# Kernel tuning notes

Measured on AMD Instinct MI355X. Metric: run time of the kernel, lower is better.

Reference implementation:

```python
import jax, jax.numpy as jnp
import numpy as np

N = 50000      # nodes
E = 800000     # edges (avg degree 16)
IN = 256       # input feature dim
H = 128        # hidden dim
L = 2          # num layers
R = 8          # NUM_RELS_WITH_MASK
RD = 16        # rel_emb_dim
CONF_W = 0.5   # conf_log_weight
LN_EPS = 1e-5


def setup_inputs() -> dict:
    key = jax.random.key(0)
    ks = jax.random.split(key, 12)
    x = jax.random.normal(ks[0], (N, IN), dtype=jnp.float32)
    edge_index = jax.random.randint(ks[1], (2, E), 0, N, dtype=jnp.int32)
    edge_type = jax.random.randint(ks[2], (E,), 0, R, dtype=jnp.int32)
    edge_attr = jax.random.uniform(ks[3], (E, 1), dtype=jnp.float32)
    # encoder input projection (Linear with bias)
    W_in = jax.random.normal(ks[4], (IN, H), dtype=jnp.float32) / np.sqrt(IN)
    b_in = jnp.zeros((H,), dtype=jnp.float32)
    # per-layer params, stacked on leading L dim
    W_msg = jax.random.normal(ks[5], (L, H, H), dtype=jnp.float32) / np.sqrt(H)
    rel_emb = jax.random.normal(ks[6], (L, R, RD), dtype=jnp.float32)
    W_rel = jax.random.normal(ks[7], (L, RD, H), dtype=jnp.float32) / np.sqrt(RD)
    att_vec = jax.random.normal(ks[8], (L, 3 * H), dtype=jnp.float32) / np.sqrt(3 * H)
    bias = jnp.zeros((L, H), dtype=jnp.float32)
    ln_g = jnp.ones((L, H), dtype=jnp.float32)
    ln_b = jnp.zeros((L, H), dtype=jnp.float32)
    return {"x": x, "edge_index": edge_index, "edge_type": edge_type,
            "edge_attr": edge_attr, "W_in": W_in, "b_in": b_in,
            "W_msg": W_msg, "rel_emb": rel_emb, "W_rel": W_rel,
            "att_vec": att_vec, "bias": bias, "ln_g": ln_g, "ln_b": ln_b}


def _layer_norm(h, g, b):
    mu = jnp.mean(h, axis=-1, keepdims=True)
    var = jnp.mean(jnp.square(h - mu), axis=-1, keepdims=True)
    return (h - mu) * jax.lax.rsqrt(var + LN_EPS) * g + b


def reference(x, edge_index, edge_type, edge_attr,
              W_in, b_in, W_msg, rel_emb, W_rel, att_vec, bias, ln_g, ln_b):
    src, dst = edge_index[0], edge_index[1]
    t = jnp.clip(edge_type, 0, R - 1)
    log_conf = CONF_W * jnp.log(jnp.maximum(edge_attr[:, 0], 1e-6))  # [E]

    h = jax.nn.relu(x @ W_in + b_in)  # [N,H]
    for l in range(L):
        # project on nodes first (same math as projecting gathered rows, E >> N)
        hm = h @ W_msg[l]                 # [N,H]
        h_src = hm[src]                   # [E,H]
        h_dst = hm[dst]                   # [E,H]
        r = rel_emb[l][t] @ W_rel[l]      # [E,H]
        a = att_vec[l]
        a_d, a_s, a_r = a[:H], a[H:2 * H], a[2 * H:]
        e = h_dst @ a_d + h_src @ a_s + r @ a_r          # [E]
        e = jax.nn.leaky_relu(e, negative_slope=0.2) + log_conf
        # segment softmax grouped by dst
        m = jax.ops.segment_max(e, dst, num_segments=N)  # [N]
        ex = jnp.exp(e - m[dst])
        s = jax.ops.segment_sum(ex, dst, num_segments=N)  # [N]
        alpha = ex / s[dst]                               # [E]
        msg = h_src * alpha[:, None]                      # [E,H]
        out = jax.ops.segment_sum(msg, dst, num_segments=N) + bias[l]
        h = _layer_norm(h + jax.nn.relu(out), ln_g[l], ln_b[l])
    return h
```

## Files before the change

kernel.cpp:

```cpp
#include <hip/hip_runtime.h>
#include <hip/hip_bf16.h>

#define N_NODES 50000
#define NE      800000
#define IN_DIM  256
#define H_DIM   128
#define NL      2
#define NR      8
#define RD_DIM  16
#define CONF_W  0.5f
#define LN_EPS  1e-5f

#define SCAN_CHUNK 1024
#define NB_SCAN    ((N_NODES + SCAN_CHUNK - 1) / SCAN_CHUNK)

typedef __attribute__((ext_vector_type(8))) short bf16x8;
typedef __attribute__((ext_vector_type(4))) float f32x4;

__device__ __forceinline__ unsigned short f2bf(float f) {
    unsigned u = __float_as_uint(f);
    u += 0x7fffu + ((u >> 16) & 1u);
    return (unsigned short)(u >> 16);
}
__device__ __forceinline__ float bf2f(unsigned short v) {
    return __uint_as_float(((unsigned)v) << 16);
}


__global__ void k_zero_counts(int* __restrict__ counts) {
    int i = blockIdx.x * 256 + threadIdx.x;
    if (i < N_NODES) counts[i] = 0;
}

__global__ void k_count(const int* __restrict__ dstv, int* __restrict__ counts,
                        int* __restrict__ rank) {
    int i = blockIdx.x * 256 + threadIdx.x;
    if (i >= NE) return;
    rank[i] = atomicAdd(counts + dstv[i], 1);
}

__global__ __launch_bounds__(256) void k_scan1(const int* __restrict__ counts,
                                               int* __restrict__ bsum) {
    __shared__ int lsum[256];
    const int t = threadIdx.x, b = blockIdx.x;
    const int base = b * SCAN_CHUNK + t * 4;
    int s = 0;
#pragma unroll
    for (int j = 0; j < 4; ++j) {
        int idx = base + j;
        if (idx < N_NODES) s += counts[idx];
    }
    lsum[t] = s;
    __syncthreads();
    for (int off = 128; off; off >>= 1) {
        if (t < off) lsum[t] += lsum[t + off];
        __syncthreads();
    }
    if (t == 0) bsum[b] = lsum[0];
}

__global__ void k_scan2(const int* __restrict__ bsum, int* __restrict__ bbase) {
    int lane = threadIdx.x & 63;
    int v = (lane < NB_SCAN) ? bsum[lane] : 0;
    int inc = v;
    for (int off = 1; off < 64; off <<= 1) {
        int tmp = __shfl_up(inc, off);
        if (lane >= off) inc += tmp;
    }
    if (lane < NB_SCAN) bbase[lane] = inc - v;
}

__global__ __launch_bounds__(256) void k_scan3(const int* __restrict__ counts,
                                               const int* __restrict__ bbase,
                                               int* __restrict__ offsets) {
    __shared__ int lsum[256];
    const int t = threadIdx.x, b = blockIdx.x;
    const int base = b * SCAN_CHUNK + t * 4;
    int c[4];
    int s = 0;
#pragma unroll
    for (int j = 0; j < 4; ++j) {
        int idx = base + j;
        c[j] = (idx < N_NODES) ? counts[idx] : 0;
        s += c[j];
    }
    lsum[t] = s;
    __syncthreads();
    for (int off = 1; off < 256; off <<= 1) {
        int v = (t >= off) ? lsum[t - off] : 0;
        __syncthreads();
        lsum[t] += v;
        __syncthreads();
    }
    int run = bbase[b] + lsum[t] - s;
#pragma unroll
    for (int j = 0; j < 4; ++j) {
        int idx = base + j;
        if (idx < N_NODES) { offsets[idx] = run; run += c[j]; }
    }
}

__global__ void k_perm(const int* __restrict__ srcv, const int* __restrict__ dstv,
                       const int* __restrict__ et, const float* __restrict__ ea,
                       const int* __restrict__ offsets, const int* __restrict__ rank,
                       int* __restrict__ src_sorted, int* __restrict__ type_sorted,
                       float* __restrict__ lc_sorted) {
    int i = blockIdx.x * 256 + threadIdx.x;
    if (i >= NE) return;
    int p = offsets[dstv[i]] + rank[i];
    src_sorted[p] = srcv[i];
    int t = et[i]; t = t < 0 ? 0 : (t > NR - 1 ? NR - 1 : t);
    type_sorted[p] = t;
    lc_sorted[p] = CONF_W * logf(fmaxf(ea[i], 1e-6f));
}

__global__ void k_rel_score(const float* __restrict__ rel_emb,
                            const float* __restrict__ W_rel,
                            const float* __restrict__ att_vec,
                            float* __restrict__ rel_score) {
    __shared__ float wvec[NL][RD_DIM];
    int t = threadIdx.x;
    if (t < NL * RD_DIM) {
        int l = t / RD_DIM, d = t % RD_DIM;
        const float* wr = W_rel + ((size_t)l * RD_DIM + d) * H_DIM;
        const float* ar = att_vec + (size_t)l * 3 * H_DIM + 2 * H_DIM;
        float s = 0.f;
        for (int k = 0; k < H_DIM; ++k) s += wr[k] * ar[k];
        wvec[l][d] = s;
    }
    __syncthreads();
    if (t < NL * NR) {
        int l = t / NR, r = t % NR;
        const float* re = rel_emb + ((size_t)l * NR + r) * RD_DIM;
        float s = 0.f;
        for (int d = 0; d < RD_DIM; ++d) s += re[d] * wvec[l][d];
        rel_score[t] = s;
    }
}

__global__ void k_cvt_weights(const float* __restrict__ W_in,
                              const float* __restrict__ W_msg,
                              unsigned short* __restrict__ Wt_in,
                              unsigned short* __restrict__ Wt_msg) {
    int i = blockIdx.x * 256 + threadIdx.x;
    if (i < H_DIM * IN_DIM) {
        int n = i >> 8, k = i & 255;
        Wt_in[i] = f2bf(W_in[(size_t)k * H_DIM + n]);
    } else if (i < H_DIM * IN_DIM + NL * H_DIM * H_DIM) {
        int r = i - H_DIM * IN_DIM;
        int l = r >> 14;
        int n = (r >> 7) & 127, k = r & 127;
        Wt_msg[r] = f2bf(W_msg[(size_t)l * H_DIM * H_DIM + (size_t)k * H_DIM + n]);
    }
}

__global__ void k_zero_scores(float* __restrict__ dsc, float* __restrict__ ssc) {
    int i = blockIdx.x * 256 + threadIdx.x;
    if (i < N_NODES) { dsc[i] = 0.f; ssc[i] = 0.f; }
}

template <int K, bool BIASRELU, bool SCORES>
__global__ __launch_bounds__(256) void k_gemm_mfma(
        const float* __restrict__ A, const unsigned short* __restrict__ Bt,
        const float* __restrict__ bias, float* __restrict__ Cf,
        unsigned short* __restrict__ Cb, int M,
        const float* __restrict__ att_vec_l,
        float* __restrict__ dsc, float* __restrict__ ssc) {
    __shared__ unsigned short As[128 * 40];
    __shared__ unsigned short Bs[128 * 40];
    const int t = threadIdx.x;
    const int wid = t >> 6, lane = t & 63;
    const int wr = wid >> 1, wc = wid & 1;
    const int lm = lane & 15, lg = lane >> 4;
    const int m0 = blockIdx.x * 128;

    f32x4 acc[4][4] = {};

    for (int k0 = 0; k0 < K; k0 += 32) {
#pragma unroll
        for (int i = 0; i < 4; ++i) {
            int flat = t + i * 256;
            int row = flat >> 3, c4 = flat & 7;
            int rm = m0 + row; rm = rm < M ? rm : M - 1;
            float4 fv = *(const float4*)(A + (size_t)rm * K + k0 + c4 * 4);
            uint2 pk;
            pk.x = (unsigned)f2bf(fv.x) | ((unsigned)f2bf(fv.y) << 16);
            pk.y = (unsigned)f2bf(fv.z) | ((unsigned)f2bf(fv.w) << 16);
            *(uint2*)(As + row * 40 + c4 * 4) = pk;
        }
#pragma unroll
        for (int i = 0; i < 2; ++i) {
            int flat = t + i * 256;
            int row = flat >> 2, ch = flat & 3;
            uint4 v = *(const uint4*)(Bt + (size_t)row * K + k0 + ch * 8);
            *(uint4*)(Bs + row * 40 + ch * 8) = v;
        }
        __syncthreads();
        bf16x8 a[4], b[4];
#pragma unroll
        for (int f = 0; f < 4; ++f) {
            a[f] = *(const bf16x8*)(As + (wr * 64 + f * 16 + lm) * 40 + lg * 8);
            b[f] = *(const bf16x8*)(Bs + (wc * 64 + f * 16 + lm) * 40 + lg * 8);
        }
#pragma unroll
        for (int fm = 0; fm < 4; ++fm)
#pragma unroll
            for (int fn = 0; fn < 4; ++fn)
                acc[fm][fn] = __builtin_amdgcn_mfma_f32_16x16x32_bf16(
                    a[fm], b[fn], acc[fm][fn], 0, 0, 0);
        __syncthreads();
    }

    float av[4], asv[4];
    if (SCORES) {
#pragma unroll
        for (int fn = 0; fn < 4; ++fn) {
            int n = wc * 64 + fn * 16 + lm;
            av[fn]  = att_vec_l[n];
            asv[fn] = att_vec_l[H_DIM + n];
        }
    }

#pragma unroll
    for (int fm = 0; fm < 4; ++fm) {
#pragma unroll
        for (int j = 0; j < 4; ++j) {
            int m = m0 + wr * 64 + fm * 16 + lg * 4 + j;
            bool valid = m < M;
            if (BIASRELU) {
#pragma unroll
                for (int fn = 0; fn < 4; ++fn) {
                    int n = wc * 64 + fn * 16 + lm;
                    float v = fmaxf(acc[fm][fn][j] + bias[n], 0.f);
                    if (valid) Cf[(size_t)m * H_DIM + n] = v;
                }
            }
            if (SCORES) {
                float pd = 0.f, ps = 0.f;
#pragma unroll
                for (int fn = 0; fn < 4; ++fn) {
                    int n = wc * 64 + fn * 16 + lm;
                    float v = acc[fm][fn][j];
                    if (valid) Cb[(size_t)m * H_DIM + n] = f2bf(v);
                    pd += v * av[fn];
                    ps += v * asv[fn];
                }
#pragma unroll
                for (int off = 8; off; off >>= 1) {
                    pd += __shfl_xor(pd, off);
                    ps += __shfl_xor(ps, off);
                }
                if (lm == 0 && valid) {
                    atomicAdd(dsc + m, pd);
                    atomicAdd(ssc + m, ps);
                }
            }
        }
    }
}

__global__ __launch_bounds__(256) void k_fused(
        const int* __restrict__ offsets, const int* __restrict__ counts,
        const int* __restrict__ src_sorted, const int* __restrict__ type_sorted,
        const float* __restrict__ lc_sorted,
        const float* __restrict__ dsc, const float* __restrict__ ssc,
        const float* __restrict__ rel_l,
        const unsigned short* __restrict__ hm, const float* __restrict__ h_in,
        const float* __restrict__ bias_l, const float* __restrict__ g,
        const float* __restrict__ b, float* __restrict__ h_out) {
    __shared__ float rel_s[NR];
    if (threadIdx.x < NR) rel_s[threadIdx.x] = rel_l[threadIdx.x];
    __syncthreads();

    const int wave = threadIdx.x >> 6, lane = threadIdx.x & 63;
    const int d = blockIdx.x * 4 + wave;
    if (d >= N_NODES) return;

    const int start = offsets[d];
    const int deg = counts[d];
    const float dsc_d = dsc[d];

    float m_l = -1e30f, s_l = 0.f;
    for (int j = lane; j < deg; j += 64) {
        int p = start + j;
        float e = dsc_d + ssc[src_sorted[p]] + rel_s[type_sorted[p]];
        e = (e > 0.f ? e : 0.2f * e) + lc_sorted[p];
        float nm = fmaxf(m_l, e);
        s_l = s_l * __expf(m_l - nm) + __expf(e - nm);
        m_l = nm;
    }
    float m = m_l;
    for (int off = 32; off; off >>= 1) m = fmaxf(m, __shfl_xor(m, off));
    float ssum = s_l * __expf(m_l - m);
    for (int off = 32; off; off >>= 1) ssum += __shfl_xor(ssum, off);

    float2 acc = make_float2(0.f, 0.f);
    const int c = 2 * lane;
    for (int k = 0; k < deg; ++k) {
        int p = start + k;
        int s = src_sorted[p];
        float e = dsc_d + ssc[s] + rel_s[type_sorted[p]];
        e = (e > 0.f ? e : 0.2f * e) + lc_sorted[p];
        float ex = __expf(e - m);
        ushort2 rv = *(const ushort2*)(hm + (size_t)s * H_DIM + c);
        acc.x += ex * bf2f(rv.x);
        acc.y += ex * bf2f(rv.y);
    }

    const float inv = (deg > 0) ? 1.f / ssum : 0.f;
    float2 bs = *(const float2*)(bias_l + c);
    float2 hi = *(const float2*)(h_in + (size_t)d * H_DIM + c);
    float v0 = hi.x + fmaxf(acc.x * inv + bs.x, 0.f);
    float v1 = hi.y + fmaxf(acc.y * inv + bs.y, 0.f);

    float sum = v0 + v1;
    for (int off = 32; off; off >>= 1) sum += __shfl_xor(sum, off);
    float mu = sum * (1.f / H_DIM);
    float d0 = v0 - mu, d1 = v1 - mu;
    float vs = d0 * d0 + d1 * d1;
    for (int off = 32; off; off >>= 1) vs += __shfl_xor(vs, off);
    float invstd = rsqrtf(vs * (1.f / H_DIM) + LN_EPS);
    float2 gg = *(const float2*)(g + c);
    float2 bb = *(const float2*)(b + c);
    float2 o;
    o.x = d0 * invstd * gg.x + bb.x;
    o.y = d1 * invstd * gg.y + bb.y;
    *(float2*)(h_out + (size_t)d * H_DIM + c) = o;
}

extern "C" void kernel_launch(void* const* d_in, const int* in_sizes, int n_in,
                              void* d_out, int out_size, void* d_ws, size_t ws_size,
                              hipStream_t stream) {
    const float* x         = (const float*)d_in[0];
    const int*   edge_index= (const int*)d_in[1];
    const int*   edge_type = (const int*)d_in[2];
    const float* edge_attr = (const float*)d_in[3];
    const float* W_in      = (const float*)d_in[4];
    const float* b_in      = (const float*)d_in[5];
    const float* W_msg     = (const float*)d_in[6];
    const float* rel_emb   = (const float*)d_in[7];
    const float* W_rel     = (const float*)d_in[8];
    const float* att_vec   = (const float*)d_in[9];
    const float* bias      = (const float*)d_in[10];
    const float* ln_g      = (const float*)d_in[11];
    const float* ln_b      = (const float*)d_in[12];
    float* out = (float*)d_out;

    char* w = (char*)d_ws;
    float* h_ws       = (float*)w; w += (size_t)N_NODES * H_DIM * 4;
    unsigned short* hm_b = (unsigned short*)w; w += (size_t)N_NODES * H_DIM * 2;
    int*   rank       = (int*)w;   w += (size_t)NE * 4;
    int*   src_sorted = (int*)w;   w += (size_t)NE * 4;
    int*   type_sorted= (int*)w;   w += (size_t)NE * 4;
    float* lc_sorted  = (float*)w; w += (size_t)NE * 4;
    int*   counts     = (int*)w;   w += (size_t)N_NODES * 4;
    int*   offsets    = (int*)w;   w += (size_t)N_NODES * 4;
    float* dsc        = (float*)w; w += (size_t)N_NODES * 4;
    float* ssc        = (float*)w; w += (size_t)N_NODES * 4;
    unsigned short* Wt_in  = (unsigned short*)w; w += (size_t)H_DIM * IN_DIM * 2;
    unsigned short* Wt_msg = (unsigned short*)w; w += (size_t)NL * H_DIM * H_DIM * 2;
    float* rel_score  = (float*)w; w += 64 * 4;
    int*   bsum       = (int*)w;   w += 64 * 4;
    int*   bbase      = (int*)w;   w += 64 * 4;

    const int* srcv = edge_index;
    const int* dstv = edge_index + NE;

    k_zero_counts<<<(N_NODES + 255) / 256, 256, 0, stream>>>(counts);
    k_count<<<(NE + 255) / 256, 256, 0, stream>>>(dstv, counts, rank);
    k_scan1<<<NB_SCAN, 256, 0, stream>>>(counts, bsum);
    k_scan2<<<1, 64, 0, stream>>>(bsum, bbase);
    k_scan3<<<NB_SCAN, 256, 0, stream>>>(counts, bbase, offsets);
    k_perm<<<(NE + 255) / 256, 256, 0, stream>>>(srcv, dstv, edge_type, edge_attr,
                                                 offsets, rank, src_sorted,
                                                 type_sorted, lc_sorted);
    k_rel_score<<<1, 256, 0, stream>>>(rel_emb, W_rel, att_vec, rel_score);
    k_cvt_weights<<<(H_DIM * IN_DIM + NL * H_DIM * H_DIM + 255) / 256, 256, 0, stream>>>(
        W_in, W_msg, Wt_in, Wt_msg);

    const int GB = (N_NODES + 127) / 128;
    k_gemm_mfma<IN_DIM, true, false><<<GB, 256, 0, stream>>>(
        x, Wt_in, b_in, h_ws, nullptr, N_NODES, nullptr, nullptr, nullptr);

    for (int l = 0; l < NL; ++l) {
        k_zero_scores<<<(N_NODES + 255) / 256, 256, 0, stream>>>(dsc, ssc);
        k_gemm_mfma<H_DIM, false, true><<<GB, 256, 0, stream>>>(
            h_ws, Wt_msg + (size_t)l * H_DIM * H_DIM, nullptr, nullptr, hm_b, N_NODES,
            att_vec + (size_t)l * 3 * H_DIM, dsc, ssc);
        k_fused<<<(N_NODES + 3) / 4, 256, 0, stream>>>(
            offsets, counts, src_sorted, type_sorted, lc_sorted, dsc, ssc,
            rel_score + l * NR, hm_b, h_ws,
            bias + (size_t)l * H_DIM, ln_g + (size_t)l * H_DIM,
            ln_b + (size_t)l * H_DIM, (l == NL - 1) ? out : h_ws);
    }
}
```

Measured before the change: 364.2 us.

## Pack edge metadata, cache edge softmax weights in LDS, feed bf16 activations to GEMM

Edge src, type and log-confidence are packed into one uint2 per edge. The src index takes 16 bits, which relies on node ids staying below 65536. The fused aggregation kernel now caches per-edge scores and src ids in shared memory for the first 128 edges per node, so the gather loop no longer recomputes scores and reloads metadata. The layer-norm and input GEMM epilogues also write a bf16 copy of h, so the message GEMM reads half the bytes and skips the conversion. Score zeroing is hoisted into a single launch over per-layer buffers, and the d>=N guard is dropped because N is divisible by 4.

```diff
diff --git a/kernel.cpp b/kernel.cpp
--- a/kernel.cpp
+++ b/kernel.cpp
@@ -13,6 +13,7 @@
 
 #define SCAN_CHUNK 1024
 #define NB_SCAN    ((N_NODES + SCAN_CHUNK - 1) / SCAN_CHUNK)
+#define DCAP       128
 
 typedef __attribute__((ext_vector_type(8))) short bf16x8;
 typedef __attribute__((ext_vector_type(4))) float f32x4;
@@ -103,15 +104,14 @@
 __global__ void k_perm(const int* __restrict__ srcv, const int* __restrict__ dstv,
                        const int* __restrict__ et, const float* __restrict__ ea,
                        const int* __restrict__ offsets, const int* __restrict__ rank,
-                       int* __restrict__ src_sorted, int* __restrict__ type_sorted,
-                       float* __restrict__ lc_sorted) {
+                       uint2* __restrict__ meta_sorted) {
     int i = blockIdx.x * 256 + threadIdx.x;
     if (i >= NE) return;
     int p = offsets[dstv[i]] + rank[i];
-    src_sorted[p] = srcv[i];
     int t = et[i]; t = t < 0 ? 0 : (t > NR - 1 ? NR - 1 : t);
-    type_sorted[p] = t;
-    lc_sorted[p] = CONF_W * logf(fmaxf(ea[i], 1e-6f));
+    float lc = CONF_W * logf(fmaxf(ea[i], 1e-6f));
+    meta_sorted[p] = make_uint2((unsigned)srcv[i] | ((unsigned)t << 16),
+                                __float_as_uint(lc));
 }
 
 __global__ void k_rel_score(const float* __restrict__ rel_emb,
@@ -156,12 +156,12 @@
 
 __global__ void k_zero_scores(float* __restrict__ dsc, float* __restrict__ ssc) {
     int i = blockIdx.x * 256 + threadIdx.x;
-    if (i < N_NODES) { dsc[i] = 0.f; ssc[i] = 0.f; }
-}
-
-template <int K, bool BIASRELU, bool SCORES>
+    if (i < NL * N_NODES) { dsc[i] = 0.f; ssc[i] = 0.f; }
+}
+
+template <int K, bool ABF16, bool BIASRELU, bool SCORES>
 __global__ __launch_bounds__(256) void k_gemm_mfma(
-        const float* __restrict__ A, const unsigned short* __restrict__ Bt,
+        const void* __restrict__ Av, const unsigned short* __restrict__ Bt,
         const float* __restrict__ bias, float* __restrict__ Cf,
         unsigned short* __restrict__ Cb, int M,
         const float* __restrict__ att_vec_l,
@@ -177,16 +177,29 @@
     f32x4 acc[4][4] = {};
 
     for (int k0 = 0; k0 < K; k0 += 32) {
-#pragma unroll
-        for (int i = 0; i < 4; ++i) {
-            int flat = t + i * 256;
-            int row = flat >> 3, c4 = flat & 7;
-            int rm = m0 + row; rm = rm < M ? rm : M - 1;
-            float4 fv = *(const float4*)(A + (size_t)rm * K + k0 + c4 * 4);
-            uint2 pk;
-            pk.x = (unsigned)f2bf(fv.x) | ((unsigned)f2bf(fv.y) << 16);
-            pk.y = (unsigned)f2bf(fv.z) | ((unsigned)f2bf(fv.w) << 16);
-            *(uint2*)(As + row * 40 + c4 * 4) = pk;
+        if (ABF16) {
+            const unsigned short* A = (const unsigned short*)Av;
+#pragma unroll
+            for (int i = 0; i < 2; ++i) {
+                int flat = t + i * 256;
+                int row = flat >> 2, ch = flat & 3;
+                int rm = m0 + row; rm = rm < M ? rm : M - 1;
+                uint4 v = *(const uint4*)(A + (size_t)rm * K + k0 + ch * 8);
+                *(uint4*)(As + row * 40 + ch * 8) = v;
+            }
+        } else {
+            const float* A = (const float*)Av;
+#pragma unroll
+            for (int i = 0; i < 4; ++i) {
+                int flat = t + i * 256;
+                int row = flat >> 3, c4 = flat & 7;
+                int rm = m0 + row; rm = rm < M ? rm : M - 1;
+                float4 fv = *(const float4*)(A + (size_t)rm * K + k0 + c4 * 4);
+                uint2 pk;
+                pk.x = (unsigned)f2bf(fv.x) | ((unsigned)f2bf(fv.y) << 16);
+                pk.y = (unsigned)f2bf(fv.z) | ((unsigned)f2bf(fv.w) << 16);
+                *(uint2*)(As + row * 40 + c4 * 4) = pk;
+            }
         }
 #pragma unroll
         for (int i = 0; i < 2; ++i) {
@@ -232,7 +245,10 @@
                 for (int fn = 0; fn < 4; ++fn) {
                     int n = wc * 64 + fn * 16 + lm;
                     float v = fmaxf(acc[fm][fn][j] + bias[n], 0.f);
-                    if (valid) Cf[(size_t)m * H_DIM + n] = v;
+                    if (valid) {
+                        Cf[(size_t)m * H_DIM + n] = v;
+                        if (Cb) Cb[(size_t)m * H_DIM + n] = f2bf(v);
+                    }
                 }
             }
             if (SCORES) {
@@ -261,50 +277,73 @@
 
 __global__ __launch_bounds__(256) void k_fused(
         const int* __restrict__ offsets, const int* __restrict__ counts,
-        const int* __restrict__ src_sorted, const int* __restrict__ type_sorted,
-        const float* __restrict__ lc_sorted,
+        const uint2* __restrict__ meta,
         const float* __restrict__ dsc, const float* __restrict__ ssc,
         const float* __restrict__ rel_l,
         const unsigned short* __restrict__ hm, const float* __restrict__ h_in,
         const float* __restrict__ bias_l, const float* __restrict__ g,
-        const float* __restrict__ b, float* __restrict__ h_out) {
+        const float* __restrict__ b, float* __restrict__ h_out,
+        unsigned short* __restrict__ h_out_bf) {
     __shared__ float rel_s[NR];
+    __shared__ float es[4][DCAP];
+    __shared__ unsigned short srcs[4][DCAP];
     if (threadIdx.x < NR) rel_s[threadIdx.x] = rel_l[threadIdx.x];
     __syncthreads();
 
     const int wave = threadIdx.x >> 6, lane = threadIdx.x & 63;
     const int d = blockIdx.x * 4 + wave;
-    if (d >= N_NODES) return;
 
     const int start = offsets[d];
     const int deg = counts[d];
     const float dsc_d = dsc[d];
 
-    float m_l = -1e30f, s_l = 0.f;
+    float m_l = -1e30f;
     for (int j = lane; j < deg; j += 64) {
-        int p = start + j;
-        float e = dsc_d + ssc[src_sorted[p]] + rel_s[type_sorted[p]];
-        e = (e > 0.f ? e : 0.2f * e) + lc_sorted[p];
-        float nm = fmaxf(m_l, e);
-        s_l = s_l * __expf(m_l - nm) + __expf(e - nm);
-        m_l = nm;
+        uint2 mv = meta[start + j];
+        int s = mv.x & 0xffff;
+        float e = dsc_d + ssc[s] + rel_s[(mv.x >> 16) & 7];
+        e = (e > 0.f ? e : 0.2f * e) + __uint_as_float(mv.y);
+        if (j < DCAP) { es[wave][j] = e; srcs[wave][j] = (unsigned short)s; }
+        m_l = fmaxf(m_l, e);
     }
     float m = m_l;
     for (int off = 32; off; off >>= 1) m = fmaxf(m, __shfl_xor(m, off));
-    float ssum = s_l * __expf(m_l - m);
+
+    float s_l = 0.f;
+    for (int j = lane; j < deg; j += 64) {
+        float e;
+        if (j < DCAP) e = es[wave][j];
+        else {
+            uint2 mv = meta[start + j];
+            e = dsc_d + ssc[mv.x & 0xffff] + rel_s[(mv.x >> 16) & 7];
+            e = (e > 0.f ? e : 0.2f * e) + __uint_as_float(mv.y);
+        }
+        float w = __expf(e - m);
+        if (j < DCAP) es[wave][j] = w;
+        s_l += w;
+    }
+    float ssum = s_l;
     for (int off = 32; off; off >>= 1) ssum += __shfl_xor(ssum, off);
+
+    __syncthreads();
 
     float2 acc = make_float2(0.f, 0.f);
     const int c = 2 * lane;
+#pragma unroll 4
     for (int k = 0; k < deg; ++k) {
-        int p = start + k;
-        int s = src_sorted[p];
-        float e = dsc_d + ssc[s] + rel_s[type_sorted[p]];
-        e = (e > 0.f ? e : 0.2f * e) + lc_sorted[p];
-        float ex = __expf(e - m);
+        float w;
+        int s;
+        if (k < DCAP) { w = es[wave][k]; s = srcs[wave][k]; }
+        else {
+            uint2 mv = meta[start + k];
+            s = mv.x & 0xffff;
+            float e = dsc_d + ssc[s] + rel_s[(mv.x >> 16) & 7];
+            e = (e > 0.f ? e : 0.2f * e) + __uint_as_float(mv.y);
+            w = __expf(e - m);
+        }
         ushort2 rv = *(const ushort2*)(hm + (size_t)s * H_DIM + c);
-        acc.x += ex * bf2f(rv.x);
-        acc.y += ex * bf2f(rv.y);
+        acc.x += w * bf2f(rv.x);
+        acc.y += w * bf2f(rv.y);
     }
 
     const float inv = (deg > 0) ? 1.f / ssum : 0.f;
@@ -326,6 +365,10 @@
     o.x = d0 * invstd * gg.x + bb.x;
     o.y = d1 * invstd * gg.y + bb.y;
     *(float2*)(h_out + (size_t)d * H_DIM + c) = o;
+    if (h_out_bf) {
+        ushort2 ob = make_ushort2(f2bf(o.x), f2bf(o.y));
+        *(ushort2*)(h_out_bf + (size_t)d * H_DIM + c) = ob;
+    }
 }
 
 extern "C" void kernel_launch(void* const* d_in, const int* in_sizes, int n_in,
@@ -348,15 +391,14 @@
 
     char* w = (char*)d_ws;
     float* h_ws       = (float*)w; w += (size_t)N_NODES * H_DIM * 4;
+    unsigned short* h_bf = (unsigned short*)w; w += (size_t)N_NODES * H_DIM * 2;
     unsigned short* hm_b = (unsigned short*)w; w += (size_t)N_NODES * H_DIM * 2;
+    uint2* meta_sorted = (uint2*)w; w += (size_t)NE * 8;
     int*   rank       = (int*)w;   w += (size_t)NE * 4;
-    int*   src_sorted = (int*)w;   w += (size_t)NE * 4;
-    int*   type_sorted= (int*)w;   w += (size_t)NE * 4;
-    float* lc_sorted  = (float*)w; w += (size_t)NE * 4;
     int*   counts     = (int*)w;   w += (size_t)N_NODES * 4;
     int*   offsets    = (int*)w;   w += (size_t)N_NODES * 4;
-    float* dsc        = (float*)w; w += (size_t)N_NODES * 4;
-    float* ssc        = (float*)w; w += (size_t)N_NODES * 4;
+    float* dsc        = (float*)w; w += (size_t)NL * N_NODES * 4;
+    float* ssc        = (float*)w; w += (size_t)NL * N_NODES * 4;
     unsigned short* Wt_in  = (unsigned short*)w; w += (size_t)H_DIM * IN_DIM * 2;
     unsigned short* Wt_msg = (unsigned short*)w; w += (size_t)NL * H_DIM * H_DIM * 2;
     float* rel_score  = (float*)w; w += 64 * 4;
@@ -372,25 +414,28 @@
     k_scan2<<<1, 64, 0, stream>>>(bsum, bbase);
     k_scan3<<<NB_SCAN, 256, 0, stream>>>(counts, bbase, offsets);
     k_perm<<<(NE + 255) / 256, 256, 0, stream>>>(srcv, dstv, edge_type, edge_attr,
-                                                 offsets, rank, src_sorted,
-                                                 type_sorted, lc_sorted);
+                                                 offsets, rank, meta_sorted);
     k_rel_score<<<1, 256, 0, stream>>>(rel_emb, W_rel, att_vec, rel_score);
     k_cvt_weights<<<(H_DIM * IN_DIM + NL * H_DIM * H_DIM + 255) / 256, 256, 0, stream>>>(
         W_in, W_msg, Wt_in, Wt_msg);
+    k_zero_scores<<<(NL * N_NODES + 255) / 256, 256, 0, stream>>>(dsc, ssc);
 
     const int GB = (N_NODES + 127) / 128;
-    k_gemm_mfma<IN_DIM, true, false><<<GB, 256, 0, stream>>>(
-        x, Wt_in, b_in, h_ws, nullptr, N_NODES, nullptr, nullptr, nullptr);
+    k_gemm_mfma<IN_DIM, false, true, false><<<GB, 256, 0, stream>>>(
+        x, Wt_in, b_in, h_ws, h_bf, N_NODES, nullptr, nullptr, nullptr);
 
     for (int l = 0; l < NL; ++l) {
-        k_zero_scores<<<(N_NODES + 255) / 256, 256, 0, stream>>>(dsc, ssc);
-        k_gemm_mfma<H_DIM, false, true><<<GB, 256, 0, stream>>>(
-            h_ws, Wt_msg + (size_t)l * H_DIM * H_DIM, nullptr, nullptr, hm_b, N_NODES,
-            att_vec + (size_t)l * 3 * H_DIM, dsc, ssc);
-        k_fused<<<(N_NODES + 3) / 4, 256, 0, stream>>>(
-            offsets, counts, src_sorted, type_sorted, lc_sorted, dsc, ssc,
+        k_gemm_mfma<H_DIM, true, false, true><<<GB, 256, 0, stream>>>(
+            h_bf, Wt_msg + (size_t)l * H_DIM * H_DIM, nullptr, nullptr, hm_b, N_NODES,
+            att_vec + (size_t)l * 3 * H_DIM, dsc + (size_t)l * N_NODES,
+            ssc + (size_t)l * N_NODES);
+        k_fused<<<N_NODES / 4, 256, 0, stream>>>(
+            offsets, counts, meta_sorted,
+            dsc + (size_t)l * N_NODES, ssc + (size_t)l * N_NODES,
             rel_score + l * NR, hm_b, h_ws,
             bias + (size_t)l * H_DIM, ln_g + (size_t)l * H_DIM,
-            ln_b + (size_t)l * H_DIM, (l == NL - 1) ? out : h_ws);
-    }
-}
+            ln_b + (size_t)l * H_DIM,
+            (l == NL - 1) ? out : h_ws,
+            (l == NL - 1) ? nullptr : h_bf);
+    }
+}
```

Result: faster. 329.8 us (-9.4%).
